# Kernel optimization log

Measured on AMD Instinct MI355X. Metric: run time of the kernel, lower is better.

The kernel has to match this reference:

```python
import jax, jax.numpy as jnp
import numpy as np

ROPE_BASE = 10000.0


def _rope_cos_sin(n, d, dtype):
    # standard llama-style rotary embedding over head dim d
    inv_freq = 1.0 / (ROPE_BASE ** (jnp.arange(0, d, 2, dtype=jnp.float32) / d))
    t = jnp.arange(n, dtype=jnp.float32)
    freqs = jnp.einsum('n,f->nf', t, inv_freq)          # [N, d/2]
    emb = jnp.concatenate([freqs, freqs], axis=-1)      # [N, d]
    return jnp.cos(emb).astype(dtype), jnp.sin(emb).astype(dtype)


def _rotate_half(x):
    x1, x2 = jnp.split(x, 2, axis=-1)
    return jnp.concatenate([-x2, x1], axis=-1)


def _apply_rope(x, cos, sin):
    # x: [B, H, N, D]; cos/sin: [N, D] broadcast over B, H
    return x * cos + _rotate_half(x) * sin


def setup_inputs() -> dict:
    key = jax.random.key(0)
    k1, k2, k3 = jax.random.split(key, 3)
    B, N, dim = 2, 2048, 1024
    heads, dim_head = 16, 64
    inner = heads * dim_head
    x = jax.random.normal(k1, (B, N, dim), dtype=jnp.float32)
    w_qkv = jax.random.normal(k2, (dim, 3 * inner), dtype=jnp.float32) * (dim ** -0.5)
    w_out = jax.random.normal(k3, (inner, dim), dtype=jnp.float32) * (inner ** -0.5)
    return {"x": x, "w_qkv": w_qkv, "w_out": w_out}


def reference(x, w_qkv, w_out):
    B, N, _ = x.shape
    heads, dim_head = 16, 64
    qkv = jnp.einsum('bnd,de->bne', x, w_qkv)
    q, k, v = jnp.split(qkv, 3, axis=-1)
    def to_heads(t):
        return t.reshape(B, N, heads, dim_head).transpose(0, 2, 1, 3)  # [B,H,N,D]
    q, k, v = to_heads(q), to_heads(k), to_heads(v)
    cos, sin = _rope_cos_sin(N, dim_head, x.dtype)
    q = _apply_rope(q, cos, sin)
    k = _apply_rope(k, cos, sin)
    scale = dim_head ** -0.5
    scores = jnp.einsum('bhqd,bhkd->bhqk', q, k) * scale   # [B,H,N,N], non-causal
    attn = jax.nn.softmax(scores, axis=-1)
    out = jnp.einsum('bhqk,bhkd->bhqd', attn, v)
    out = out.transpose(0, 2, 1, 3).reshape(B, N, heads * dim_head)
    return jnp.einsum('bne,ed->bnd', out, w_out)
```

## Files before the change

### kernel.cpp

```cpp
#include <hip/hip_runtime.h>

typedef __attribute__((ext_vector_type(8))) short bf16x8;
typedef __attribute__((ext_vector_type(4))) float f32x4;

#define MFMA(a, b, c) __builtin_amdgcn_mfma_f32_16x16x32_bf16(a, b, c, 0, 0, 0)

__device__ __forceinline__ unsigned short f2bf(float f) {
    unsigned u = __builtin_bit_cast(unsigned, f);
    u += 0x7fffu + ((u >> 16) & 1u);
    return (unsigned short)(u >> 16);
}

__device__ __forceinline__ void gload16(const unsigned short* g, unsigned short* l) {
    __builtin_amdgcn_global_load_lds(
        (const __attribute__((address_space(1))) void*)g,
        (__attribute__((address_space(3))) void*)l, 16, 0, 0);
}


__global__ __launch_bounds__(256) void cvt_bf16(const float* __restrict__ in,
                                                unsigned short* __restrict__ out, int n) {
    int i = (blockIdx.x * 256 + threadIdx.x) * 4;
    if (i < n) {
        float4 f = *(const float4*)(in + i);
        ushort4 u;
        u.x = f2bf(f.x); u.y = f2bf(f.y); u.z = f2bf(f.z); u.w = f2bf(f.w);
        *(ushort4*)(out + i) = u;
    }
}

__global__ __launch_bounds__(256) void transpose_cvt(const float* __restrict__ in,
                                                     unsigned short* __restrict__ out,
                                                     int R, int C) {
    __shared__ float tile[32][33];
    const int c0 = blockIdx.x * 32, r0 = blockIdx.y * 32;
    const int tr = threadIdx.x >> 3;
    const int j4 = (threadIdx.x & 7) * 4;
    float4 f = *(const float4*)(in + (size_t)(r0 + tr) * C + c0 + j4);
    tile[tr][j4 + 0] = f.x; tile[tr][j4 + 1] = f.y;
    tile[tr][j4 + 2] = f.z; tile[tr][j4 + 3] = f.w;
    __syncthreads();
    ushort4 u;
    u.x = f2bf(tile[j4 + 0][tr]); u.y = f2bf(tile[j4 + 1][tr]);
    u.z = f2bf(tile[j4 + 2][tr]); u.w = f2bf(tile[j4 + 3][tr]);
    *(ushort4*)(out + (size_t)(c0 + tr) * R + r0 + j4) = u;
}

__global__ __launch_bounds__(256) void rope_tab(float* __restrict__ cosT,
                                                float* __restrict__ sinT) {
    int i = blockIdx.x * 256 + threadIdx.x;
    int n = i >> 5, f = i & 31;
    float ang = (float)n * exp2f((float)f * -0.4152410118609203f);
    float s, c;
    sincosf(ang, &s, &c);
    cosT[i] = c; sinT[i] = s;
}


template <int EPI>
__global__ __launch_bounds__(256, 2) void gemm_bt(const unsigned short* __restrict__ A,
                                                  const unsigned short* __restrict__ Bt,
                                                  int K, int Ncols,
                                                  unsigned short* __restrict__ oq,
                                                  unsigned short* __restrict__ ok,
                                                  unsigned short* __restrict__ ovt,
                                                  float* __restrict__ of,
                                                  const float* __restrict__ cosT,
                                                  const float* __restrict__ sinT) {
    __shared__ unsigned short As[128 * 40];
    __shared__ unsigned short Bs[128 * 40];
    const int tid = threadIdx.x;
    const int w = tid >> 6, lane = tid & 63, quad = lane >> 4, cc = lane & 15;
    const int wm = w >> 1, wn = w & 1;
    const int m0 = blockIdx.y * 128, n0 = blockIdx.x * 128;

    f32x4 acc[4][4] = {};
    const int srow = tid >> 1, shalf = tid & 1;
    const size_t arow = (size_t)(m0 + srow) * K;
    const size_t brow = (size_t)(n0 + srow) * K;

    for (int kt = 0; kt < K; kt += 32) {
        uint4 a0 = *(const uint4*)(A + arow + kt + shalf * 16);
        uint4 a1 = *(const uint4*)(A + arow + kt + shalf * 16 + 8);
        uint4 b0 = *(const uint4*)(Bt + brow + kt + shalf * 16);
        uint4 b1 = *(const uint4*)(Bt + brow + kt + shalf * 16 + 8);
        __syncthreads();
        *(uint4*)&As[srow * 40 + shalf * 16 + 0] = a0;
        *(uint4*)&As[srow * 40 + shalf * 16 + 8] = a1;
        *(uint4*)&Bs[srow * 40 + shalf * 16 + 0] = b0;
        *(uint4*)&Bs[srow * 40 + shalf * 16 + 8] = b1;
        __syncthreads();
        bf16x8 af[4], bf[4];
#pragma unroll
        for (int i = 0; i < 4; i++)
            af[i] = *(const bf16x8*)&As[(wm * 64 + i * 16 + cc) * 40 + quad * 8];
#pragma unroll
        for (int i = 0; i < 4; i++)
            bf[i] = *(const bf16x8*)&Bs[(wn * 64 + i * 16 + cc) * 40 + quad * 8];
#pragma unroll
        for (int i = 0; i < 4; i++)
#pragma unroll
            for (int j = 0; j < 4; j++)
                acc[i][j] = MFMA(af[i], bf[j], acc[i][j]);
    }

    if (EPI == 0) {
        const int e0 = n0 + wn * 64;
        const int which = e0 >> 10;
        const int h = (e0 >> 6) & 15;
        if (which < 2) {
            unsigned short* dst = (which == 0) ? oq : ok;
            const float postscale = (which == 0) ? 0.125f : 1.0f;
#pragma unroll
            for (int mf = 0; mf < 4; mf++) {
#pragma unroll
                for (int r = 0; r < 4; r++) {
                    int mg = m0 + wm * 64 + mf * 16 + quad * 4 + r;
                    int nseq = mg & 2047, b = mg >> 11;
                    float vals[4];
#pragma unroll
                    for (int nf = 0; nf < 4; nf++) vals[nf] = acc[mf][nf][r];
                    size_t rowbase = ((size_t)(b * 16 + h) * 2048 + nseq) * 64;
#pragma unroll
                    for (int nf = 0; nf < 4; nf++) {
                        int d = nf * 16 + cc;
                        int f = d & 31;
                        float cs = cosT[nseq * 32 + f];
                        float sn = sinT[nseq * 32 + f];
                        float partner = vals[nf ^ 2];
                        float outv = (vals[nf] * cs +
                                      ((nf < 2) ? -partner : partner) * sn) * postscale;
                        dst[rowbase + d] = f2bf(outv);
                    }
                }
            }
        } else {
#pragma unroll
            for (int mf = 0; mf < 4; mf++) {
                int mg0 = m0 + wm * 64 + mf * 16 + quad * 4;
                int b = mg0 >> 11, nseq = mg0 & 2047;
#pragma unroll
                for (int nf = 0; nf < 4; nf++) {
                    int d = nf * 16 + cc;
                    ushort4 pk;
                    pk.x = f2bf(acc[mf][nf][0]);
                    pk.y = f2bf(acc[mf][nf][1]);
                    pk.z = f2bf(acc[mf][nf][2]);
                    pk.w = f2bf(acc[mf][nf][3]);
                    *(ushort4*)(ovt + ((size_t)(b * 16 + h) * 64 + d) * 2048 + nseq) = pk;
                }
            }
        }
    } else {
#pragma unroll
        for (int mf = 0; mf < 4; mf++)
#pragma unroll
            for (int nf = 0; nf < 4; nf++)
#pragma unroll
                for (int r = 0; r < 4; r++) {
                    int mg = m0 + wm * 64 + mf * 16 + quad * 4 + r;
                    of[(size_t)mg * Ncols + n0 + wn * 64 + nf * 16 + cc] = acc[mf][nf][r];
                }
    }
}


__global__ __launch_bounds__(256, 2) void attn(const unsigned short* __restrict__ q,
                                               const unsigned short* __restrict__ k,
                                               const unsigned short* __restrict__ vt,
                                               unsigned short* __restrict__ o) {
    __shared__ unsigned short ks[2][64 * 64];
    __shared__ unsigned short vs[2][64 * 64];
    __shared__ unsigned short ps[128 * 72];
    const int tid = threadIdx.x;
    const int w = tid >> 6, lane = tid & 63, quad = lane >> 4, cc = lane & 15;
    const int bh = blockIdx.x & 31, qt = blockIdx.x >> 5;

    const unsigned short* qg = q + ((size_t)bh * 2048 + qt * 128 + w * 32) * 64;
    bf16x8 aq[2][2];
#pragma unroll
    for (int mf = 0; mf < 2; mf++)
#pragma unroll
        for (int kc = 0; kc < 2; kc++)
            aq[mf][kc] = *(const bf16x8*)(qg + (mf * 16 + cc) * 64 + kc * 32 + quad * 8);

    int koff[2], voff[2];
#pragma unroll
    for (int t = 0; t < 2; t++) {
        int S = w * 128 + t * 64 + lane;
        int row = S >> 3;
        int c = (S & 7) ^ (row & 7);
        koff[t] = row * 64 + c * 8;
        voff[t] = row * 2048 + c * 8;
    }

    const unsigned short* kg0 = k + (size_t)bh * 2048 * 64;
    const unsigned short* vg0 = vt + (size_t)bh * 64 * 2048;

#pragma unroll
    for (int t = 0; t < 2; t++) {
        gload16(kg0 + koff[t], &ks[0][(w * 2 + t) * 512]);
        gload16(vg0 + voff[t], &vs[0][(w * 2 + t) * 512]);
    }
    __syncthreads();

    f32x4 oacc[2][4] = {};
    float rs[2][4] = {};

    for (int kt = 0; kt < 32; kt++) {
        const int pb = kt & 1;
        if (kt < 31) {
            const unsigned short* kb = kg0 + (kt + 1) * 4096;
            const unsigned short* vb = vg0 + (kt + 1) * 64;
#pragma unroll
            for (int t = 0; t < 2; t++) {
                gload16(kb + koff[t], &ks[pb ^ 1][(w * 2 + t) * 512]);
                gload16(vb + voff[t], &vs[pb ^ 1][(w * 2 + t) * 512]);
            }
        }

        f32x4 s[2][4] = {};
#pragma unroll
        for (int kc = 0; kc < 2; kc++) {
#pragma unroll
            for (int nf = 0; nf < 4; nf++) {
                bf16x8 bk = *(const bf16x8*)&ks[pb][(nf * 16 + cc) * 64 +
                                                    ((kc * 4 + quad) ^ (cc & 7)) * 8];
                s[0][nf] = MFMA(aq[0][kc], bk, s[0][nf]);
                s[1][nf] = MFMA(aq[1][kc], bk, s[1][nf]);
            }
        }

#pragma unroll
        for (int mf = 0; mf < 2; mf++)
#pragma unroll
            for (int nf = 0; nf < 4; nf++)
#pragma unroll
                for (int r = 0; r < 4; r++) {
                    float p = __builtin_amdgcn_exp2f(
                        __builtin_fmaf(s[mf][nf][r], 1.44269504f, -11.54156036f));
                    rs[mf][r] += p;
                    ps[(w * 32 + mf * 16 + quad * 4 + r) * 72 + nf * 16 + cc] = f2bf(p);
                }

#pragma unroll
        for (int kc = 0; kc < 2; kc++) {
            bf16x8 ap[2];
            ap[0] = *(const bf16x8*)&ps[(w * 32 + cc) * 72 + kc * 32 + quad * 8];
            ap[1] = *(const bf16x8*)&ps[(w * 32 + 16 + cc) * 72 + kc * 32 + quad * 8];
#pragma unroll
            for (int df = 0; df < 4; df++) {
                bf16x8 bv = *(const bf16x8*)&vs[pb][(df * 16 + cc) * 64 +
                                                    ((kc * 4 + quad) ^ (cc & 7)) * 8];
                oacc[0][df] = MFMA(ap[0], bv, oacc[0][df]);
                oacc[1][df] = MFMA(ap[1], bv, oacc[1][df]);
            }
        }

        __syncthreads();
    }

#pragma unroll
    for (int mf = 0; mf < 2; mf++)
#pragma unroll
        for (int r = 0; r < 4; r++)
#pragma unroll
            for (int off = 1; off < 16; off <<= 1)
                rs[mf][r] += __shfl_xor(rs[mf][r], off, 64);

#pragma unroll
    for (int mf = 0; mf < 2; mf++)
#pragma unroll
        for (int r = 0; r < 4; r++) {
            float inv = 1.0f / rs[mf][r];
#pragma unroll
            for (int df = 0; df < 4; df++)
                ps[(w * 32 + mf * 16 + quad * 4 + r) * 72 + df * 16 + cc] =
                    f2bf(oacc[mf][df][r] * inv);
        }
    __syncthreads();
    {
        const int b = bh >> 4, h = bh & 15;
        int row = tid >> 1, hf = tid & 1;
        unsigned short* og =
            o + ((size_t)(b * 2048 + qt * 128 + row)) * 1024 + h * 64 + hf * 32;
#pragma unroll
        for (int j = 0; j < 4; j++)
            *(uint4*)(og + j * 8) = *(const uint4*)&ps[row * 72 + hf * 32 + j * 8];
    }
}


extern "C" void kernel_launch(void* const* d_in, const int* in_sizes, int n_in,
                              void* d_out, int out_size, void* d_ws, size_t ws_size,
                              hipStream_t stream) {
    const float* x = (const float*)d_in[0];
    const float* w_qkv = (const float*)d_in[1];
    const float* w_out = (const float*)d_in[2];
    float* out = (float*)d_out;

    unsigned short* xb    = (unsigned short*)d_ws;
    unsigned short* wqkvT = xb + 4096 * 1024;
    unsigned short* woutT = wqkvT + 3072 * 1024;
    unsigned short* qb    = woutT + 1024 * 1024;
    unsigned short* kb    = qb + 2 * 16 * 2048 * 64;
    unsigned short* vtb   = kb + 2 * 16 * 2048 * 64;
    unsigned short* ob    = vtb + 2 * 16 * 2048 * 64;
    float* cosT = (float*)(ob + 4096 * 1024);
    float* sinT = cosT + 2048 * 32;

    rope_tab<<<256, 256, 0, stream>>>(cosT, sinT);
    cvt_bf16<<<4096, 256, 0, stream>>>(x, xb, 4096 * 1024);
    transpose_cvt<<<dim3(96, 32), 256, 0, stream>>>(w_qkv, wqkvT, 1024, 3072);
    transpose_cvt<<<dim3(32, 32), 256, 0, stream>>>(w_out, woutT, 1024, 1024);
    gemm_bt<0><<<dim3(24, 32), 256, 0, stream>>>(xb, wqkvT, 1024, 3072,
                                                 qb, kb, vtb, nullptr, cosT, sinT);
    attn<<<512, 256, 0, stream>>>(qb, kb, vtb, ob);
    gemm_bt<1><<<dim3(8, 32), 256, 0, stream>>>(ob, woutT, 1024, 1024,
                                                nullptr, nullptr, nullptr, out,
                                                nullptr, nullptr);
}
```

Measured before the change: 213.7 us.

## Double-buffer GEMM with async LDS loads and transpose attention score MFMA

The GEMM now uses global_load_lds to prefetch the next K tile into a double-buffered, XOR-swizzled shared-memory layout. This replaces the register-staged load with two barriers per iteration, and launch bounds are raised to 3 blocks per SM. In the attention kernel the QK^T MFMA operands are swapped so each lane holds 4 consecutive key columns of one query row. That allows packed bf16 stores of P and a row-sum reduced over only 2 shuffle steps, with the final normalisation redistributed through a small LDS buffer. Packing now rounds half-up instead of to nearest-even, and the higher occupancy target may raise register pressure or spill in the GEMM.

```diff
diff --git a/kernel.cpp b/kernel.cpp
--- a/kernel.cpp
+++ b/kernel.cpp
@@ -15,6 +15,12 @@
     __builtin_amdgcn_global_load_lds(
         (const __attribute__((address_space(1))) void*)g,
         (__attribute__((address_space(3))) void*)l, 16, 0, 0);
+}
+
+__device__ __forceinline__ unsigned pack_bf16(float lo, float hi) {
+    unsigned a = __builtin_bit_cast(unsigned, lo) + 0x8000u;
+    unsigned b = __builtin_bit_cast(unsigned, hi) + 0x8000u;
+    return __builtin_amdgcn_perm(b, a, 0x07060302);
 }
 
 
@@ -58,7 +64,7 @@
 
 
 template <int EPI>
-__global__ __launch_bounds__(256, 2) void gemm_bt(const unsigned short* __restrict__ A,
+__global__ __launch_bounds__(256, 3) void gemm_bt(const unsigned short* __restrict__ A,
                                                   const unsigned short* __restrict__ Bt,
                                                   int K, int Ncols,
                                                   unsigned short* __restrict__ oq,
@@ -67,41 +73,57 @@
                                                   float* __restrict__ of,
                                                   const float* __restrict__ cosT,
                                                   const float* __restrict__ sinT) {
-    __shared__ unsigned short As[128 * 40];
-    __shared__ unsigned short Bs[128 * 40];
+    __shared__ unsigned short As[2][128 * 32];
+    __shared__ unsigned short Bs[2][128 * 32];
     const int tid = threadIdx.x;
     const int w = tid >> 6, lane = tid & 63, quad = lane >> 4, cc = lane & 15;
     const int wm = w >> 1, wn = w & 1;
     const int m0 = blockIdx.y * 128, n0 = blockIdx.x * 128;
 
+    size_t aoff[2], boff[2];
+#pragma unroll
+    for (int t = 0; t < 2; t++) {
+        int S = w * 128 + t * 64 + lane;
+        int row = S >> 2;
+        int c = (S & 3) ^ ((row >> 1) & 3);
+        aoff[t] = (size_t)(m0 + row) * K + c * 8;
+        boff[t] = (size_t)(n0 + row) * K + c * 8;
+    }
+
+#pragma unroll
+    for (int t = 0; t < 2; t++) {
+        gload16(A + aoff[t], &As[0][(w * 2 + t) * 512]);
+        gload16(Bt + boff[t], &Bs[0][(w * 2 + t) * 512]);
+    }
+    __syncthreads();
+
     f32x4 acc[4][4] = {};
-    const int srow = tid >> 1, shalf = tid & 1;
-    const size_t arow = (size_t)(m0 + srow) * K;
-    const size_t brow = (size_t)(n0 + srow) * K;
-
-    for (int kt = 0; kt < K; kt += 32) {
-        uint4 a0 = *(const uint4*)(A + arow + kt + shalf * 16);
-        uint4 a1 = *(const uint4*)(A + arow + kt + shalf * 16 + 8);
-        uint4 b0 = *(const uint4*)(Bt + brow + kt + shalf * 16);
-        uint4 b1 = *(const uint4*)(Bt + brow + kt + shalf * 16 + 8);
-        __syncthreads();
-        *(uint4*)&As[srow * 40 + shalf * 16 + 0] = a0;
-        *(uint4*)&As[srow * 40 + shalf * 16 + 8] = a1;
-        *(uint4*)&Bs[srow * 40 + shalf * 16 + 0] = b0;
-        *(uint4*)&Bs[srow * 40 + shalf * 16 + 8] = b1;
-        __syncthreads();
+    const int rpos = (quad ^ ((cc >> 1) & 3)) * 8;
+    const int nkt = K >> 5;
+
+    for (int kt = 0; kt < nkt; kt++) {
+        const int pb = kt & 1;
+        if (kt < nkt - 1) {
+            const int ko = (kt + 1) * 32;
+#pragma unroll
+            for (int t = 0; t < 2; t++) {
+                gload16(A + aoff[t] + ko, &As[pb ^ 1][(w * 2 + t) * 512]);
+                gload16(Bt + boff[t] + ko, &Bs[pb ^ 1][(w * 2 + t) * 512]);
+            }
+        }
         bf16x8 af[4], bf[4];
 #pragma unroll
         for (int i = 0; i < 4; i++)
-            af[i] = *(const bf16x8*)&As[(wm * 64 + i * 16 + cc) * 40 + quad * 8];
+            af[i] = *(const bf16x8*)&As[pb][(wm * 64 + i * 16 + cc) * 32 + rpos];
 #pragma unroll
         for (int i = 0; i < 4; i++)
-            bf[i] = *(const bf16x8*)&Bs[(wn * 64 + i * 16 + cc) * 40 + quad * 8];
+            bf[i] = *(const bf16x8*)&Bs[pb][(wn * 64 + i * 16 + cc) * 32 + rpos];
 #pragma unroll
         for (int i = 0; i < 4; i++)
 #pragma unroll
             for (int j = 0; j < 4; j++)
                 acc[i][j] = MFMA(af[i], bf[j], acc[i][j]);
+        __syncthreads();
     }
 
     if (EPI == 0) {
@@ -172,6 +194,7 @@
     __shared__ unsigned short ks[2][64 * 64];
     __shared__ unsigned short vs[2][64 * 64];
     __shared__ unsigned short ps[128 * 72];
+    __shared__ float rsb[128];
     const int tid = threadIdx.x;
     const int w = tid >> 6, lane = tid & 63, quad = lane >> 4, cc = lane & 15;
     const int bh = blockIdx.x & 31, qt = blockIdx.x >> 5;
@@ -205,7 +228,7 @@
     __syncthreads();
 
     f32x4 oacc[2][4] = {};
-    float rs[2][4] = {};
+    float rs[2] = {};
 
     for (int kt = 0; kt < 32; kt++) {
         const int pb = kt & 1;
@@ -219,29 +242,37 @@
             }
         }
 
-        f32x4 s[2][4] = {};
+        f32x4 s2[2][4] = {};
 #pragma unroll
         for (int kc = 0; kc < 2; kc++) {
 #pragma unroll
             for (int nf = 0; nf < 4; nf++) {
                 bf16x8 bk = *(const bf16x8*)&ks[pb][(nf * 16 + cc) * 64 +
                                                     ((kc * 4 + quad) ^ (cc & 7)) * 8];
-                s[0][nf] = MFMA(aq[0][kc], bk, s[0][nf]);
-                s[1][nf] = MFMA(aq[1][kc], bk, s[1][nf]);
-            }
-        }
-
-#pragma unroll
-        for (int mf = 0; mf < 2; mf++)
-#pragma unroll
-            for (int nf = 0; nf < 4; nf++)
-#pragma unroll
-                for (int r = 0; r < 4; r++) {
-                    float p = __builtin_amdgcn_exp2f(
-                        __builtin_fmaf(s[mf][nf][r], 1.44269504f, -11.54156036f));
-                    rs[mf][r] += p;
-                    ps[(w * 32 + mf * 16 + quad * 4 + r) * 72 + nf * 16 + cc] = f2bf(p);
-                }
+                s2[0][nf] = MFMA(bk, aq[0][kc], s2[0][nf]);
+                s2[1][nf] = MFMA(bk, aq[1][kc], s2[1][nf]);
+            }
+        }
+
+#pragma unroll
+        for (int mf = 0; mf < 2; mf++) {
+#pragma unroll
+            for (int nf = 0; nf < 4; nf++) {
+                float p0 = __builtin_amdgcn_exp2f(
+                    __builtin_fmaf(s2[mf][nf][0], 1.44269504f, -11.54156036f));
+                float p1 = __builtin_amdgcn_exp2f(
+                    __builtin_fmaf(s2[mf][nf][1], 1.44269504f, -11.54156036f));
+                float p2 = __builtin_amdgcn_exp2f(
+                    __builtin_fmaf(s2[mf][nf][2], 1.44269504f, -11.54156036f));
+                float p3 = __builtin_amdgcn_exp2f(
+                    __builtin_fmaf(s2[mf][nf][3], 1.44269504f, -11.54156036f));
+                rs[mf] += (p0 + p1) + (p2 + p3);
+                uint2 pk;
+                pk.x = pack_bf16(p0, p1);
+                pk.y = pack_bf16(p2, p3);
+                *(uint2*)&ps[(w * 32 + mf * 16 + cc) * 72 + nf * 16 + quad * 4] = pk;
+            }
+        }
 
 #pragma unroll
         for (int kc = 0; kc < 2; kc++) {
@@ -261,23 +292,28 @@
     }
 
 #pragma unroll
-    for (int mf = 0; mf < 2; mf++)
+    for (int mf = 0; mf < 2; mf++) {
+        rs[mf] += __shfl_xor(rs[mf], 16, 64);
+        rs[mf] += __shfl_xor(rs[mf], 32, 64);
+    }
+    if (quad == 0) {
+        rsb[w * 32 + cc] = rs[0];
+        rsb[w * 32 + 16 + cc] = rs[1];
+    }
+
+#pragma unroll
+    for (int mf = 0; mf < 2; mf++) {
+        f32x4 rv = *(const f32x4*)&rsb[w * 32 + mf * 16 + quad * 4];
+        f32x4 inv;
+#pragma unroll
+        for (int r = 0; r < 4; r++) inv[r] = 1.0f / rv[r];
 #pragma unroll
         for (int r = 0; r < 4; r++)
-#pragma unroll
-            for (int off = 1; off < 16; off <<= 1)
-                rs[mf][r] += __shfl_xor(rs[mf][r], off, 64);
-
-#pragma unroll
-    for (int mf = 0; mf < 2; mf++)
-#pragma unroll
-        for (int r = 0; r < 4; r++) {
-            float inv = 1.0f / rs[mf][r];
 #pragma unroll
             for (int df = 0; df < 4; df++)
                 ps[(w * 32 + mf * 16 + quad * 4 + r) * 72 + df * 16 + cc] =
-                    f2bf(oacc[mf][df][r] * inv);
-        }
+                    f2bf(oacc[mf][df][r] * inv[r]);
+    }
     __syncthreads();
     {
         const int b = bh >> 4, h = bh & 15;
```

After: 190.3 us. -11.0%, faster.
